# Optimization experiments

Hardware: AMD Instinct MI355X
Metric: run time of the kernel (lower is better)

The kernel has to match this reference:

```python
import jax, jax.numpy as jnp
import numpy as np

SEQ, B, I, H = 512, 64, 1024, 1024
P_DROP = 0.1

def setup_inputs() -> dict:
    key = jax.random.key(0)
    ks = jax.random.split(key, 6)
    x = jax.random.normal(ks[0], (SEQ, B, I), dtype=jnp.float32)
    # deterministic dropout keep-mask (1.0 = keep), Bernoulli(1-p)
    keep_mask = (jax.random.uniform(ks[1], (SEQ, B, H)) > P_DROP).astype(jnp.float32)
    s_in = 1.0 / np.sqrt(H)
    W_ih = jax.random.normal(ks[2], (4 * H, I), dtype=jnp.float32) * s_in
    W_hh = jax.random.normal(ks[3], (4 * H, H), dtype=jnp.float32) * s_in
    b_ih = jax.random.normal(ks[4], (4 * H,), dtype=jnp.float32) * s_in
    b_hh = jax.random.normal(ks[5], (4 * H,), dtype=jnp.float32) * s_in
    return {"x": x, "keep_mask": keep_mask, "W_ih": W_ih, "W_hh": W_hh,
            "b_ih": b_ih, "b_hh": b_hh, "training": 1}

def reference(x, keep_mask, W_ih, W_hh, b_ih, b_hh, training):
    # PyTorch LSTMCell: gates in i, f, g, o order; stepwise inverted dropout on h.
    scale = 1.0 / (1.0 - P_DROP) if training else 1.0
    Hh = W_hh.shape[1]

    def step(carry, inp):
        h, c = carry
        xt, mt = inp  # [B,I], [B,H]
        gates = xt @ W_ih.T + b_ih + h @ W_hh.T + b_hh  # [B,4H]
        i_g, f_g, g_g, o_g = jnp.split(gates, 4, axis=-1)
        i_g = jax.nn.sigmoid(i_g)
        f_g = jax.nn.sigmoid(f_g)
        g_g = jnp.tanh(g_g)
        o_g = jax.nn.sigmoid(o_g)
        c = f_g * c + i_g * g_g
        h = o_g * jnp.tanh(c)
        if training:
            h = h * mt * scale  # stepwise dropout, dropped h fed to next step
        return (h, c), None

    h0 = jnp.zeros((x.shape[1], Hh), dtype=x.dtype)
    c0 = jnp.zeros_like(h0)
    (h, _), _ = jax.lax.scan(step, (h0, c0), (x, keep_mask))
    return h  # [B, H] final (dropped) hidden state
```

## Files before the change

### kernel.cpp

```cpp
#include <hip/hip_runtime.h>
#include <hip/hip_bf16.h>

typedef __bf16 bf16x8 __attribute__((ext_vector_type(8)));
typedef float  f32x4  __attribute__((ext_vector_type(4)));
typedef unsigned short u16;
typedef unsigned int   u32;

#define SEQ   512
#define BATCH 64
#define INP   1024
#define HID   1024
#define NREC  64
#define NGRID 256

#define WC_OFF    0ull
#define HSEQ_OFF  (WC_OFF + 16777216ull)
#define BIAS_OFF  (HSEQ_OFF + 67239936ull)
#define FLAGS_OFF (BIAS_OFF + 16384ull)

__device__ __forceinline__ u16 f2bf(float f) {
    u32 u = __float_as_uint(f);
    u = (u + 0x7FFFu + ((u >> 16) & 1u)) >> 16;
    return (u16)u;
}

__device__ __forceinline__ bf16x8 ld8(const u16* p) {
    return *reinterpret_cast<const bf16x8*>(p);
}

__device__ __forceinline__ bf16x8 cvt8(const float* p) {
    float4 lo = *reinterpret_cast<const float4*>(p);
    float4 hi = *reinterpret_cast<const float4*>(p + 4);
    union { __hip_bfloat162 h2[4]; bf16x8 v; } u;
    u.h2[0] = __float22bfloat162_rn(float2{lo.x, lo.y});
    u.h2[1] = __float22bfloat162_rn(float2{lo.z, lo.w});
    u.h2[2] = __float22bfloat162_rn(float2{hi.x, hi.y});
    u.h2[3] = __float22bfloat162_rn(float2{hi.z, hi.w});
    return u.v;
}

__device__ __forceinline__ float sigmoidf_fast(float x) {
    return 1.0f / (1.0f + __expf(-x));
}
__device__ __forceinline__ float tanhf_fast(float x) {
    return 2.0f / (1.0f + __expf(-2.0f * x)) - 1.0f;
}

__global__ void lstm_prep(const float* __restrict__ wih,
                          const float* __restrict__ whh,
                          const float* __restrict__ bih,
                          const float* __restrict__ bhh,
                          u16* __restrict__ wc, u16* __restrict__ hseq,
                          float* __restrict__ bias, u32* __restrict__ flags) {
    const long long NW = 8388608ll;
    const long long NB = 4096ll;
    const long long NH = 65536ll;
    const long long NF = 2080ll;
    const long long total = NW + NB + NH + NF;
    long long stride = (long long)gridDim.x * blockDim.x;
    for (long long i = (long long)blockIdx.x * blockDim.x + threadIdx.x;
         i < total; i += stride) {
        if (i < NW) {
            long long row = i >> 11;
            long long col = i & 2047;
            float v = (col < 1024) ? wih[row * 1024 + col]
                                   : whh[row * 1024 + (col - 1024)];
            wc[i] = f2bf(v);
        } else if (i < NW + NB) {
            long long j = i - NW;
            bias[j] = bih[j] + bhh[j];
        } else if (i < NW + NB + NH) {
            hseq[i - NW - NB] = 0;
        } else {
            flags[i - NW - NB - NH] = 0;
        }
    }
}

__global__ __launch_bounds__(256, 1) void lstm_rec(
    const float* __restrict__ x, const u16* __restrict__ wc,
    const float* __restrict__ bias, const float* __restrict__ km,
    u16* __restrict__ hseq, float* __restrict__ out,
    u32* __restrict__ flags, const int* __restrict__ trainp) {

    __shared__ float part[4][4][BATCH][16];

    const int tid = threadIdx.x;

    if (blockIdx.x >= NREC) {
        volatile int* mb = (volatile int*)&part[0][0][0][0];
        if (tid == 0) *mb = 0;
        __syncthreads();
        union { u32 u[4]; bf16x8 v; } ja, jb;
        #pragma unroll
        for (int i = 0; i < 4; ++i) {
            ja.u[i] = (u32)tid * 2654435761u + i;
            jb.u[i] = (u32)tid * 40503u + 7u * i + 1u;
        }
        f32x4 hacc[8];
        #pragma unroll
        for (int j = 0; j < 8; ++j) hacc[j] = (f32x4){0.f, 0.f, 0.f, 0.f};
        const u32* done = flags + 2048;
        for (int chunk = 0; chunk < 4096; ++chunk) {
            #pragma unroll 1
            for (int it = 0; it < 256; ++it) {
                #pragma unroll
                for (int j = 0; j < 8; ++j)
                    hacc[j] = __builtin_amdgcn_mfma_f32_16x16x32_bf16(
                        ja.v, jb.v, hacc[j], 0, 0, 0);
            }
            if (tid < 64) {
                u32 d = __hip_atomic_load(done, __ATOMIC_RELAXED,
                                          __HIP_MEMORY_SCOPE_AGENT);
                if (d) *mb = 1;
            }
            if (*mb) break;
        }
        float s = 0.f;
        #pragma unroll
        for (int j = 0; j < 8; ++j)
            s += hacc[j][0] + hacc[j][1] + hacc[j][2] + hacc[j][3];
        asm volatile("" :: "v"(s));
        return;
    }

    const int w    = tid >> 6;
    const int lane = tid & 63;
    const int quad = lane >> 4;
    const int l16  = lane & 15;
    const int cu   = blockIdx.x;
    const int col0 = cu * 16;

    const int training = trainp[0];
    const float scale = training ? (1.0f / 0.9f) : 1.0f;

    const u16* wbase = wc + (size_t)(col0 + l16) * 2048 + (size_t)w * 256
                          + (size_t)quad * 8;

    const int cj2 = (tid & 7) * 2;
    const int cb0 = tid >> 3;
    float bi[4][2];
    #pragma unroll
    for (int g = 0; g < 4; ++g) {
        bi[g][0] = bias[g * 1024 + col0 + cj2];
        bi[g][1] = bias[g * 1024 + col0 + cj2 + 1];
    }

    float creg[2][2] = {{0.f, 0.f}, {0.f, 0.f}};

    #pragma unroll 1
    for (int t = 0; t < SEQ; ++t) {
        float2 kmv[2];
        kmv[0] = *reinterpret_cast<const float2*>(
            &km[(size_t)t * 65536 + (size_t)cb0 * 1024 + col0 + cj2]);
        kmv[1] = *reinterpret_cast<const float2*>(
            &km[(size_t)t * 65536 + (size_t)(cb0 + 32) * 1024 + col0 + cj2]);

        f32x4 acc[4][4];
        #pragma unroll
        for (int g = 0; g < 4; ++g)
            #pragma unroll
            for (int mt = 0; mt < 4; ++mt)
                acc[g][mt] = (f32x4){0.f, 0.f, 0.f, 0.f};

        {
            const float* Arow = x + (size_t)t * (BATCH * INP)
                                  + (size_t)l16 * 1024 + (size_t)w * 256
                                  + (size_t)quad * 8;
            #pragma unroll 4
            for (int kk = 0; kk < 8; ++kk) {
                bf16x8 afr[4], bfr[4];
                #pragma unroll
                for (int mt = 0; mt < 4; ++mt)
                    afr[mt] = cvt8(Arow + (size_t)mt * 16 * 1024 + kk * 32);
                #pragma unroll
                for (int g = 0; g < 4; ++g)
                    bfr[g] = ld8(wbase + (size_t)g * 1024 * 2048 + kk * 32);
                #pragma unroll
                for (int g = 0; g < 4; ++g)
                    #pragma unroll
                    for (int mt = 0; mt < 4; ++mt)
                        acc[g][mt] = __builtin_amdgcn_mfma_f32_16x16x32_bf16(
                            afr[mt], bfr[g], acc[g][mt], 0, 0, 0);
            }
        }

        if (t > 0) {
            const u32* fl = flags + ((u32)lane << 5);
            while (true) {
                u32 f = __hip_atomic_load(fl, __ATOMIC_RELAXED,
                                          __HIP_MEMORY_SCOPE_AGENT);
                if (__ballot((int)f >= t) == 0xFFFFFFFFFFFFFFFFull) break;
                __builtin_amdgcn_s_sleep(1);
            }
            asm volatile("" ::: "memory");
        }

        {
            const u16* Hrow = hseq + (size_t)t * 65536
                                   + (size_t)l16 * 1024 + (size_t)w * 256
                                   + (size_t)quad * 8;
            #pragma unroll 4
            for (int kk = 0; kk < 8; ++kk) {
                bf16x8 afr[4], bfr[4];
                #pragma unroll
                for (int mt = 0; mt < 4; ++mt)
                    afr[mt] = ld8(Hrow + (size_t)mt * 16 * 1024 + kk * 32);
                #pragma unroll
                for (int g = 0; g < 4; ++g)
                    bfr[g] = ld8(wbase + 1024 + (size_t)g * 1024 * 2048 + kk * 32);
                #pragma unroll
                for (int g = 0; g < 4; ++g)
                    #pragma unroll
                    for (int mt = 0; mt < 4; ++mt)
                        acc[g][mt] = __builtin_amdgcn_mfma_f32_16x16x32_bf16(
                            afr[mt], bfr[g], acc[g][mt], 0, 0, 0);
            }
        }

        #pragma unroll
        for (int g = 0; g < 4; ++g)
            #pragma unroll
            for (int mt = 0; mt < 4; ++mt)
                #pragma unroll
                for (int r = 0; r < 4; ++r)
                    part[w][g][mt * 16 + quad * 4 + r][l16] = acc[g][mt][r];

        __syncthreads();

        u16* hout = hseq + (size_t)(t + 1) * 65536;
        #pragma unroll
        for (int r = 0; r < 2; ++r) {
            int b = cb0 + 32 * r;
            float hv[2];
            #pragma unroll
            for (int c = 0; c < 2; ++c) {
                int j = cj2 + c;
                float gi = part[0][0][b][j] + part[1][0][b][j]
                         + part[2][0][b][j] + part[3][0][b][j] + bi[0][c];
                float gf = part[0][1][b][j] + part[1][1][b][j]
                         + part[2][1][b][j] + part[3][1][b][j] + bi[1][c];
                float gg = part[0][2][b][j] + part[1][2][b][j]
                         + part[2][2][b][j] + part[3][2][b][j] + bi[2][c];
                float go = part[0][3][b][j] + part[1][3][b][j]
                         + part[2][3][b][j] + part[3][3][b][j] + bi[3][c];

                float ig = sigmoidf_fast(gi);
                float fg = sigmoidf_fast(gf);
                float gt = tanhf_fast(gg);
                float og = sigmoidf_fast(go);

                float cv = fg * creg[r][c] + ig * gt;
                creg[r][c] = cv;
                float h = og * tanhf_fast(cv);
                if (training)
                    h = h * (c ? kmv[r].y : kmv[r].x) * scale;
                hv[c] = h;
            }
            int cidx = b * 1024 + col0 + cj2;
            u32 packed = (u32)f2bf(hv[0]) | ((u32)f2bf(hv[1]) << 16);
            __hip_atomic_store((u32*)(hout + cidx), packed,
                               __ATOMIC_RELAXED, __HIP_MEMORY_SCOPE_AGENT);
            if (t == SEQ - 1) {
                out[cidx]     = hv[0];
                out[cidx + 1] = hv[1];
            }
        }

        asm volatile("s_waitcnt vmcnt(0)" ::: "memory");
        __syncthreads();
        if (tid == 0) {
            __hip_atomic_store(flags + ((u32)cu << 5), (u32)(t + 1),
                               __ATOMIC_RELAXED, __HIP_MEMORY_SCOPE_AGENT);
        }
    }

    if (cu == 0 && tid == 0) {
        __hip_atomic_store(flags + 2048, 1u,
                           __ATOMIC_RELAXED, __HIP_MEMORY_SCOPE_AGENT);
    }
}

extern "C" void kernel_launch(void* const* d_in, const int* in_sizes, int n_in,
                              void* d_out, int out_size, void* d_ws, size_t ws_size,
                              hipStream_t stream) {
    const float* x   = (const float*)d_in[0];
    const float* km  = (const float*)d_in[1];
    const float* wih = (const float*)d_in[2];
    const float* whh = (const float*)d_in[3];
    const float* bih = (const float*)d_in[4];
    const float* bhh = (const float*)d_in[5];
    const int*   tr  = (const int*)d_in[6];
    float* out = (float*)d_out;

    char* ws = (char*)d_ws;
    u16*   wc    = (u16*)(ws + WC_OFF);
    u16*   hseq  = (u16*)(ws + HSEQ_OFF);
    float* bias  = (float*)(ws + BIAS_OFF);
    u32*   flags = (u32*)(ws + FLAGS_OFF);

    lstm_prep<<<dim3(1024), dim3(256), 0, stream>>>(wih, whh, bih, bhh,
                                                    wc, hseq, bias, flags);
    lstm_rec<<<dim3(NGRID), dim3(256), 0, stream>>>(x, wc, bias, km, hseq,
                                                    out, flags, tr);
}
```

Measured before the change: 11.12 ms.

## Keep recurrent W_hh fragments in registers across timesteps; make idle blocks spin on FMA

The recurrent blocks now load their slice of W_hh into registers (8x4 bf16x8 vectors) once before the time loop. Previously they reloaded those fragments from global memory every step on the serial critical path. The inner k loop is fully unrolled to use the preloaded fragments. The idle 'heater' blocks replace their MFMA busy loop with a scalar FMA chain, which may reduce contention or power draw while the recurrent blocks run. Holding 128 extra VGPRs per thread raises register pressure and could cause spills.

```diff
diff --git a/kernel.cpp b/kernel.cpp
--- a/kernel.cpp
+++ b/kernel.cpp
@@ -91,36 +91,28 @@
         volatile int* mb = (volatile int*)&part[0][0][0][0];
         if (tid == 0) *mb = 0;
         __syncthreads();
-        union { u32 u[4]; bf16x8 v; } ja, jb;
-        #pragma unroll
-        for (int i = 0; i < 4; ++i) {
-            ja.u[i] = (u32)tid * 2654435761u + i;
-            jb.u[i] = (u32)tid * 40503u + 7u * i + 1u;
-        }
-        f32x4 hacc[8];
-        #pragma unroll
-        for (int j = 0; j < 8; ++j) hacc[j] = (f32x4){0.f, 0.f, 0.f, 0.f};
+        float a0 = (float)tid * 1e-7f + 1.0f;
+        float a1 = a0 + 0.25f;
+        float a2 = a0 + 0.50f;
+        float a3 = a0 + 0.75f;
+        const float m = 1.0000001f, d = 1e-9f;
         const u32* done = flags + 2048;
-        for (int chunk = 0; chunk < 4096; ++chunk) {
+        for (int chunk = 0; chunk < 65536; ++chunk) {
             #pragma unroll 1
-            for (int it = 0; it < 256; ++it) {
-                #pragma unroll
-                for (int j = 0; j < 8; ++j)
-                    hacc[j] = __builtin_amdgcn_mfma_f32_16x16x32_bf16(
-                        ja.v, jb.v, hacc[j], 0, 0, 0);
+            for (int it = 0; it < 1024; ++it) {
+                a0 = __builtin_fmaf(a0, m, d);
+                a1 = __builtin_fmaf(a1, m, d);
+                a2 = __builtin_fmaf(a2, m, d);
+                a3 = __builtin_fmaf(a3, m, d);
             }
             if (tid < 64) {
-                u32 d = __hip_atomic_load(done, __ATOMIC_RELAXED,
-                                          __HIP_MEMORY_SCOPE_AGENT);
-                if (d) *mb = 1;
+                u32 dn = __hip_atomic_load(done, __ATOMIC_RELAXED,
+                                           __HIP_MEMORY_SCOPE_AGENT);
+                if (dn) *mb = 1;
             }
             if (*mb) break;
         }
-        float s = 0.f;
-        #pragma unroll
-        for (int j = 0; j < 8; ++j)
-            s += hacc[j][0] + hacc[j][1] + hacc[j][2] + hacc[j][3];
-        asm volatile("" :: "v"(s));
+        asm volatile("" :: "v"(a0 + a1 + a2 + a3));
         return;
     }
 
@@ -146,6 +138,13 @@
         bi[g][1] = bias[g * 1024 + col0 + cj2 + 1];
     }
 
+    bf16x8 whr[8][4];
+    #pragma unroll
+    for (int kk = 0; kk < 8; ++kk)
+        #pragma unroll
+        for (int g = 0; g < 4; ++g)
+            whr[kk][g] = ld8(wbase + 1024 + (size_t)g * 1024 * 2048 + kk * 32);
+
     float creg[2][2] = {{0.f, 0.f}, {0.f, 0.f}};
 
     #pragma unroll 1
@@ -200,21 +199,18 @@
             const u16* Hrow = hseq + (size_t)t * 65536
                                    + (size_t)l16 * 1024 + (size_t)w * 256
                                    + (size_t)quad * 8;
-            #pragma unroll 4
+            #pragma unroll
             for (int kk = 0; kk < 8; ++kk) {
-                bf16x8 afr[4], bfr[4];
+                bf16x8 afr[4];
                 #pragma unroll
                 for (int mt = 0; mt < 4; ++mt)
                     afr[mt] = ld8(Hrow + (size_t)mt * 16 * 1024 + kk * 32);
-                #pragma unroll
-                for (int g = 0; g < 4; ++g)
-                    bfr[g] = ld8(wbase + 1024 + (size_t)g * 1024 * 2048 + kk * 32);
                 #pragma unroll
                 for (int g = 0; g < 4; ++g)
                     #pragma unroll
                     for (int mt = 0; mt < 4; ++mt)
                         acc[g][mt] = __builtin_amdgcn_mfma_f32_16x16x32_bf16(
-                            afr[mt], bfr[g], acc[g][mt], 0, 0, 0);
+                            afr[mt], whr[kk][g], acc[g][mt], 0, 0, 0);
             }
         }
 
```

Measured after the change: 13.31 ms. +19.7%, slower.
